# Kernel tuning notes

Measured on AMD Instinct MI355X. Metric: run time of the kernel, lower is better.

The kernel has to match this reference:

```python
import jax, jax.numpy as jnp
import numpy as np

D = 256
N_CELL = 100000
N_NET = 50000
E = 300000
EPS = 1e-5


def _agg_mean(src_feat, edge_index, num_dst):
    # edge_index[0]=src, edge_index[1]=dst; gather + segment-sum + degree-normalize
    src_idx, dst_idx = edge_index[0], edge_index[1]
    summed = jax.ops.segment_sum(src_feat[src_idx], dst_idx, num_segments=num_dst)
    deg = jax.ops.segment_sum(jnp.ones((src_idx.shape[0], 1), src_feat.dtype), dst_idx, num_segments=num_dst)
    return summed / jnp.maximum(deg, 1.0)


def _mlp(x, w1, b1, w2, b2):
    return jax.nn.relu(x @ w1 + b1) @ w2 + b2


def _layernorm(x, g, b):
    mu = jnp.mean(x, axis=-1, keepdims=True)
    var = jnp.var(x, axis=-1, keepdims=True)
    return (x - mu) * jax.lax.rsqrt(var + EPS) * g + b


def setup_inputs() -> dict:
    key = jax.random.key(0)
    ks = jax.random.split(key, 24)
    inp = {
        'cell_h': jax.random.normal(ks[0], (N_CELL, D), jnp.float32),
        'net_h': jax.random.normal(ks[1], (N_NET, D), jnp.float32),
        'cell_to_net_edge_index': jax.random.randint(ks[2], (2, E), 0, 50000),
        'net_to_cell_edge_index': jax.random.randint(ks[3], (2, E), 0, 50000),
        'cell_to_cell_edge_index': jax.random.randint(ks[4], (2, E), 0, 50000),
    }
    def lin(k, fin, fout):
        return jax.random.normal(k, (fin, fout), jnp.float32) * 0.02
    for i, name in enumerate(['c2n', 'n2c', 'c2c']):
        inp[name + '_w1'] = lin(ks[5 + 4 * i], 2 * D, D)
        inp[name + '_b1'] = jnp.zeros((D,), jnp.float32)
        inp[name + '_w2'] = lin(ks[6 + 4 * i], D, D)
        inp[name + '_b2'] = jnp.zeros((D,), jnp.float32)
    inp['net_ln_g'] = jnp.ones((D,), jnp.float32)
    inp['net_ln_b'] = jnp.zeros((D,), jnp.float32)
    inp['cell_ln_g'] = jnp.ones((D,), jnp.float32)
    inp['cell_ln_b'] = jnp.zeros((D,), jnp.float32)
    return inp


def reference(cell_h, net_h, cell_to_net_edge_index, net_to_cell_edge_index,
              cell_to_cell_edge_index,
              c2n_w1, c2n_b1, c2n_w2, c2n_b2,
              n2c_w1, n2c_b1, n2c_w2, n2c_b2,
              c2c_w1, c2c_b1, c2c_w2, c2c_b2,
              net_ln_g, net_ln_b, cell_ln_g, cell_ln_b):
    # cells -> nets
    msg_c2n = _agg_mean(cell_h, cell_to_net_edge_index, net_h.shape[0])
    net_h = _layernorm(net_h + _mlp(jnp.concatenate([net_h, msg_c2n], axis=-1),
                                    c2n_w1, c2n_b1, c2n_w2, c2n_b2),
                       net_ln_g, net_ln_b)
    # nets -> cells
    msg_n2c = _agg_mean(net_h, net_to_cell_edge_index, cell_h.shape[0])
    cell_h = cell_h + _mlp(jnp.concatenate([cell_h, msg_n2c], axis=-1),
                           n2c_w1, n2c_b1, n2c_w2, n2c_b2)
    # cells -> cells
    msg_c2c = _agg_mean(cell_h, cell_to_cell_edge_index, cell_h.shape[0])
    cell_h = cell_h + _mlp(jnp.concatenate([cell_h, msg_c2c], axis=-1),
                           c2c_w1, c2c_b1, c2c_w2, c2c_b2)
    cell_h = _layernorm(cell_h, cell_ln_g, cell_ln_b)
    return (cell_h, net_h)
```

## Files before the change

kernel.cpp:

```cpp
#include <hip/hip_runtime.h>
#include <stdint.h>

typedef unsigned short u16;
typedef short short8 __attribute__((ext_vector_type(8)));
typedef short short4v __attribute__((ext_vector_type(4)));
typedef float floatx4 __attribute__((ext_vector_type(4)));

#define D_FEAT 256

__device__ __forceinline__ u16 f2bf(float x){
  unsigned u = __float_as_uint(x);
  u += 0x7FFFu + ((u >> 16) & 1u);
  return (u16)(u >> 16);
}

__device__ __forceinline__ short8 pack8(float4 a, float4 b){
  short8 v;
  v[0]=(short)f2bf(a.x); v[1]=(short)f2bf(a.y); v[2]=(short)f2bf(a.z); v[3]=(short)f2bf(a.w);
  v[4]=(short)f2bf(b.x); v[5]=(short)f2bf(b.y); v[6]=(short)f2bf(b.z); v[7]=(short)f2bf(b.w);
  return v;
}

__global__ void conv_t_kernel(const float* __restrict__ w, u16* __restrict__ wt, int K, int N){
  int idx = blockIdx.x * 256 + threadIdx.x;
  if (idx >= K * N) return;
  int k = idx / N, n = idx - k * N;
  wt[(size_t)n * K + k] = f2bf(w[idx]);
}

__global__ void hist_kernel(const int* __restrict__ didx, int E, int* __restrict__ cnt){
  int e = blockIdx.x * 256 + threadIdx.x;
  if (e < E) atomicAdd(&cnt[didx[e]], 1);
}

__global__ void scan_block_kernel(const int* __restrict__ cnt, int* __restrict__ excl,
                                  int* __restrict__ bsums, int N){
  __shared__ int tmp[256];
  int t = threadIdx.x;
  int i = blockIdx.x * 256 + t;
  int v = (i < N) ? cnt[i] : 0;
  tmp[t] = v; __syncthreads();
#pragma unroll
  for (int o = 1; o < 256; o <<= 1){
    int x = (t >= o) ? tmp[t - o] : 0;
    __syncthreads();
    tmp[t] += x;
    __syncthreads();
  }
  if (i < N) excl[i] = tmp[t] - v;
  if (t == 255) bsums[blockIdx.x] = tmp[255];
}

__global__ void scan_bsums_kernel(int* __restrict__ bsums, int nb){
  __shared__ int tmp[512];
  int t = threadIdx.x;
  if (nb > 512){
    if (t == 0){
      int acc = 0;
      for (int i = 0; i < nb; i++){ int v = bsums[i]; bsums[i] = acc; acc += v; }
    }
    return;
  }
  int v = (t < nb) ? bsums[t] : 0;
  tmp[t] = v; __syncthreads();
#pragma unroll
  for (int o = 1; o < 512; o <<= 1){
    int x = (t >= o) ? tmp[t - o] : 0;
    __syncthreads();
    tmp[t] += x;
    __syncthreads();
  }
  if (t < nb) bsums[t] = tmp[t] - v;
}

__global__ void scan_add_kernel(int* __restrict__ excl, const int* __restrict__ bsums, int N){
  int i = blockIdx.x * 256 + threadIdx.x;
  if (i < N) excl[i] += bsums[blockIdx.x];
}

__global__ void fill_csr_kernel(const int* __restrict__ sidx, const int* __restrict__ didx, int E,
                                const int* __restrict__ row_start, int* __restrict__ fillc,
                                int* __restrict__ esrc){
  int e = blockIdx.x * 256 + threadIdx.x;
  if (e >= E) return;
  int d = didx[e];
  int pos = atomicAdd(&fillc[d], 1);
  esrc[row_start[d] + pos] = sidx[e];
}

__global__ void agg_mean_kernel(const float* __restrict__ feat, const int* __restrict__ row_start,
                                const int* __restrict__ cnt, const int* __restrict__ esrc,
                                u16* __restrict__ mean, int M){
  int row = blockIdx.x * 4 + (threadIdx.x >> 6);
  int lane = threadIdx.x & 63;
  if (row >= M) return;
  int beg = row_start[row], n = cnt[row];
  float4 a0 = {0.f,0.f,0.f,0.f}, a1 = {0.f,0.f,0.f,0.f};
  int j = 0;
  for (; j + 1 < n; j += 2){
    int s0 = esrc[beg + j], s1 = esrc[beg + j + 1];
    float4 v0 = ((const float4*)(feat + (size_t)s0 * D_FEAT))[lane];
    float4 v1 = ((const float4*)(feat + (size_t)s1 * D_FEAT))[lane];
    a0.x += v0.x; a0.y += v0.y; a0.z += v0.z; a0.w += v0.w;
    a1.x += v1.x; a1.y += v1.y; a1.z += v1.z; a1.w += v1.w;
  }
  if (j < n){
    int s0 = esrc[beg + j];
    float4 v0 = ((const float4*)(feat + (size_t)s0 * D_FEAT))[lane];
    a0.x += v0.x; a0.y += v0.y; a0.z += v0.z; a0.w += v0.w;
  }
  float inv = 1.0f / fmaxf((float)n, 1.0f);
  short4v o;
  o[0] = (short)f2bf((a0.x + a1.x) * inv);
  o[1] = (short)f2bf((a0.y + a1.y) * inv);
  o[2] = (short)f2bf((a0.z + a1.z) * inv);
  o[3] = (short)f2bf((a0.w + a1.w) * inv);
  ((short4v*)(mean + (size_t)row * D_FEAT))[lane] = o;
}

template<int HAS_LN>
__global__ __launch_bounds__(256, 3) void fused_mlp_kernel(
    const float* __restrict__ h, const u16* __restrict__ s,
    const u16* __restrict__ B1t, const float* __restrict__ b1,
    const u16* __restrict__ B2t, const float* __restrict__ b2,
    const float* __restrict__ resid,
    const float* __restrict__ lng, const float* __restrict__ lnb,
    float* __restrict__ out, int M)
{
  __shared__ __align__(16) char smem_raw[53248];
  short8* As8 = (short8*)smem_raw;
  short8* Bs8 = (short8*)(smem_raw + 4096);
  u16*    hid = (u16*)(smem_raw + 20480);
  float*  part = (float*)smem_raw;

  int tid = threadIdx.x;
  int wave = tid >> 6, lane = tid & 63;
  int half = lane >> 4, l16 = lane & 15;
  int wc = wave * 64;
  int row0 = blockIdx.x * 64;

  int rA = tid >> 2, uA = tid & 3;
  int rgA = row0 + rA;
  int aw_idx = (rA << 2) | (uA ^ (rA & 3));

  floatx4 acc[4][4];
  floatx4 zero4 = {0.f, 0.f, 0.f, 0.f};
#pragma unroll
  for (int i = 0; i < 4; i++)
#pragma unroll
    for (int j = 0; j < 4; j++) acc[i][j] = zero4;

  float4 pa0 = {0.f,0.f,0.f,0.f}, pa1 = {0.f,0.f,0.f,0.f};
  short8 ps = {0,0,0,0,0,0,0,0};
  short8 pbv[4];

  {
    int kk = uA * 8;
    if (rgA < M){
      const float* src = h + (size_t)rgA * 256 + kk;
      pa0 = ((const float4*)src)[0];
      pa1 = ((const float4*)src)[1];
    }
#pragma unroll
    for (int cc = 0; cc < 4; cc++){
      int c = tid + cc * 256;
      int r = c >> 2, u = c & 3;
      pbv[cc] = *(const short8*)(B1t + (size_t)r * 512 + u * 8);
    }
  }

  for (int k0 = 0; k0 < 512; k0 += 32){
    {
      short8 va = {0,0,0,0,0,0,0,0};
      if (k0 < 256){ if (rgA < M) va = pack8(pa0, pa1); }
      else         { va = ps; }
      As8[aw_idx] = va;
    }
#pragma unroll
    for (int cc = 0; cc < 4; cc++){
      int c = tid + cc * 256;
      int r = c >> 2, u = c & 3;
      Bs8[(r << 2) | (u ^ (r & 3))] = pbv[cc];
    }
    __syncthreads();

    if (k0 < 480){
      int k0n = k0 + 32;
      int kk = k0n + uA * 8;
      if (k0n < 256){
        if (rgA < M){
          const float* src = h + (size_t)rgA * 256 + kk;
          pa0 = ((const float4*)src)[0];
          pa1 = ((const float4*)src)[1];
        }
      } else {
        ps = (rgA < M) ? *(const short8*)(s + (size_t)rgA * 256 + (kk - 256))
                       : (short8){0,0,0,0,0,0,0,0};
      }
#pragma unroll
      for (int cc = 0; cc < 4; cc++){
        int c = tid + cc * 256;
        int r = c >> 2, u = c & 3;
        pbv[cc] = *(const short8*)(B1t + (size_t)r * 512 + k0n + u * 8);
      }
    }

    short8 af[4], bfr[4];
#pragma unroll
    for (int t = 0; t < 4; t++){
      int ra = t * 16 + l16;
      af[t] = As8[(ra << 2) | (half ^ (ra & 3))];
      int rb = wc + t * 16 + l16;
      bfr[t] = Bs8[(rb << 2) | (half ^ (rb & 3))];
    }
#pragma unroll
    for (int i = 0; i < 4; i++)
#pragma unroll
      for (int j = 0; j < 4; j++)
        acc[i][j] = __builtin_amdgcn_mfma_f32_16x16x32_bf16(af[i], bfr[j], acc[i][j], 0, 0, 0);
    __syncthreads();
  }

#pragma unroll
  for (int i = 0; i < 4; i++){
#pragma unroll
    for (int j = 0; j < 4; j++){
      int cg = wc + j * 16 + l16;
      float bv = b1[cg];
#pragma unroll
      for (int r = 0; r < 4; r++){
        int lr = i * 16 + half * 4 + r;
        int idx = lr * 256 + ((((cg >> 3) ^ (lr & 7)) << 3) | (cg & 7));
        hid[idx] = f2bf(fmaxf(acc[i][j][r] + bv, 0.0f));
      }
    }
  }

#pragma unroll
  for (int i = 0; i < 4; i++)
#pragma unroll
    for (int j = 0; j < 4; j++) acc[i][j] = zero4;

#pragma unroll
  for (int cc = 0; cc < 4; cc++){
    int c = tid + cc * 256;
    int r = c >> 2, u = c & 3;
    pbv[cc] = *(const short8*)(B2t + (size_t)r * 256 + u * 8);
  }

  for (int k0 = 0; k0 < 256; k0 += 32){
#pragma unroll
    for (int cc = 0; cc < 4; cc++){
      int c = tid + cc * 256;
      int r = c >> 2, u = c & 3;
      Bs8[(r << 2) | (u ^ (r & 3))] = pbv[cc];
    }
    __syncthreads();

    if (k0 < 224){
      int k0n = k0 + 32;
#pragma unroll
      for (int cc = 0; cc < 4; cc++){
        int c = tid + cc * 256;
        int r = c >> 2, u = c & 3;
        pbv[cc] = *(const short8*)(B2t + (size_t)r * 256 + k0n + u * 8);
      }
    }

    short8 af[4], bfr[4];
#pragma unroll
    for (int t = 0; t < 4; t++){
      int ra = t * 16 + l16;
      int chunkL = (k0 >> 3) + half;
      af[t] = *(const short8*)(hid + ra * 256 + ((chunkL ^ (ra & 7)) << 3));
      int rb = wc + t * 16 + l16;
      bfr[t] = Bs8[(rb << 2) | (half ^ (rb & 3))];
    }
#pragma unroll
    for (int i = 0; i < 4; i++)
#pragma unroll
      for (int j = 0; j < 4; j++)
        acc[i][j] = __builtin_amdgcn_mfma_f32_16x16x32_bf16(af[i], bfr[j], acc[i][j], 0, 0, 0);
    __syncthreads();
  }

#pragma unroll
  for (int i = 0; i < 4; i++){
#pragma unroll
    for (int j = 0; j < 4; j++){
      int cg = wc + j * 16 + l16;
      float bv = b2[cg];
#pragma unroll
      for (int r = 0; r < 4; r++){
        int lr = i * 16 + half * 4 + r;
        int rg = row0 + lr;
        float rv = (rg < M) ? resid[(size_t)rg * 256 + cg] : 0.0f;
        acc[i][j][r] = acc[i][j][r] + bv + rv;
      }
    }
  }

  if (HAS_LN){
#pragma unroll
    for (int i = 0; i < 4; i++){
#pragma unroll
      for (int r = 0; r < 4; r++){
        float s1 = 0.f, s2 = 0.f;
#pragma unroll
        for (int j = 0; j < 4; j++){
          float v = acc[i][j][r];
          s1 += v; s2 += v * v;
        }
#pragma unroll
        for (int m = 1; m < 16; m <<= 1){
          s1 += __shfl_xor(s1, m, 64);
          s2 += __shfl_xor(s2, m, 64);
        }
        if (l16 == 0){
          int lr = i * 16 + half * 4 + r;
          part[lr * 4 + wave]       = s1;
          part[256 + lr * 4 + wave] = s2;
        }
      }
    }
    __syncthreads();
#pragma unroll
    for (int i = 0; i < 4; i++){
#pragma unroll
      for (int r = 0; r < 4; r++){
        int lr = i * 16 + half * 4 + r;
        int rg = row0 + lr;
        float4 p1 = *(const float4*)(part + lr * 4);
        float4 p2 = *(const float4*)(part + 256 + lr * 4);
        float su = p1.x + p1.y + p1.z + p1.w;
        float sq = p2.x + p2.y + p2.z + p2.w;
        float mean = su * (1.0f / 256.0f);
        float var = sq * (1.0f / 256.0f) - mean * mean;
        float rs = rsqrtf(var + 1e-5f);
        if (rg < M){
#pragma unroll
          for (int j = 0; j < 4; j++){
            int cg = wc + j * 16 + l16;
            float vv = (acc[i][j][r] - mean) * rs * lng[cg] + lnb[cg];
            out[(size_t)rg * 256 + cg] = vv;
          }
        }
      }
    }
  } else {
#pragma unroll
    for (int i = 0; i < 4; i++){
#pragma unroll
      for (int r = 0; r < 4; r++){
        int lr = i * 16 + half * 4 + r;
        int rg = row0 + lr;
        if (rg < M){
#pragma unroll
          for (int j = 0; j < 4; j++){
            int cg = wc + j * 16 + l16;
            out[(size_t)rg * 256 + cg] = acc[i][j][r];
          }
        }
      }
    }
  }
}

static void run_agg(const float* feat, const int* edge, int E, int Ndst,
                    int* cnt, int* row_start, int* fillc, int* bsums, int* esrc,
                    u16* mean, hipStream_t stream){
  const int* sidx = edge;
  const int* didx = edge + E;
  hipMemsetAsync(cnt, 0, (size_t)Ndst * 4, stream);
  hipMemsetAsync(fillc, 0, (size_t)Ndst * 4, stream);
  int egrid = (E + 255) / 256;
  hist_kernel<<<egrid, 256, 0, stream>>>(didx, E, cnt);
  int nb = (Ndst + 255) / 256;
  scan_block_kernel<<<nb, 256, 0, stream>>>(cnt, row_start, bsums, Ndst);
  scan_bsums_kernel<<<1, 512, 0, stream>>>(bsums, nb);
  scan_add_kernel<<<nb, 256, 0, stream>>>(row_start, bsums, Ndst);
  fill_csr_kernel<<<egrid, 256, 0, stream>>>(sidx, didx, E, row_start, fillc, esrc);
  agg_mean_kernel<<<(Ndst + 3) / 4, 256, 0, stream>>>(feat, row_start, cnt, esrc, mean, Ndst);
}

extern "C" void kernel_launch(void* const* d_in, const int* in_sizes, int n_in,
                              void* d_out, int out_size, void* d_ws, size_t ws_size,
                              hipStream_t stream){
  const float* cell_h = (const float*)d_in[0];
  const float* net_h  = (const float*)d_in[1];
  const int* e_c2n = (const int*)d_in[2];
  const int* e_n2c = (const int*)d_in[3];
  const int* e_c2c = (const int*)d_in[4];
  const float* w1p[3] = {(const float*)d_in[5], (const float*)d_in[9],  (const float*)d_in[13]};
  const float* b1p[3] = {(const float*)d_in[6], (const float*)d_in[10], (const float*)d_in[14]};
  const float* w2p[3] = {(const float*)d_in[7], (const float*)d_in[11], (const float*)d_in[15]};
  const float* b2p[3] = {(const float*)d_in[8], (const float*)d_in[12], (const float*)d_in[16]};
  const float* net_g  = (const float*)d_in[17];
  const float* net_b  = (const float*)d_in[18];
  const float* cell_g = (const float*)d_in[19];
  const float* cell_b = (const float*)d_in[20];

  int n_cell = in_sizes[0] / 256;
  int n_net  = in_sizes[1] / 256;
  int E = in_sizes[2] / 2;

  float* cell_out = (float*)d_out;
  float* net_out  = (float*)d_out + (size_t)n_cell * 256;

  char* p = (char*)d_ws;
  u16* w1t[3]; u16* w2t[3];
  for (int i = 0; i < 3; i++){
    w1t[i] = (u16*)p; p += (size_t)512 * 256 * 2;
    w2t[i] = (u16*)p; p += (size_t)256 * 256 * 2;
  }
  u16* Mbuf = (u16*)p; p += (size_t)n_cell * 256 * 2;
  int n_pad = ((n_cell + 63) / 64) * 64;
  int* cnt       = (int*)p; p += (size_t)n_pad * 4;
  int* row_start = (int*)p; p += (size_t)n_pad * 4;
  int* fillc     = (int*)p; p += (size_t)n_pad * 4;
  int* bsums     = (int*)p; p += 1024 * 4;
  int* esrc      = (int*)p; p += (size_t)E * 4;

  for (int i = 0; i < 3; i++){
    conv_t_kernel<<<(512 * 256 + 255) / 256, 256, 0, stream>>>(w1p[i], w1t[i], 512, 256);
    conv_t_kernel<<<(256 * 256 + 255) / 256, 256, 0, stream>>>(w2p[i], w2t[i], 256, 256);
  }

  dim3 blk(256);

  run_agg(cell_h, e_c2n, E, n_net, cnt, row_start, fillc, bsums, esrc, Mbuf, stream);
  fused_mlp_kernel<1><<<dim3((n_net + 63) / 64), blk, 0, stream>>>(
      net_h, Mbuf, w1t[0], b1p[0], w2t[0], b2p[0], net_h, net_g, net_b, net_out, n_net);

  run_agg(net_out, e_n2c, E, n_cell, cnt, row_start, fillc, bsums, esrc, Mbuf, stream);
  fused_mlp_kernel<0><<<dim3((n_cell + 63) / 64), blk, 0, stream>>>(
      cell_h, Mbuf, w1t[1], b1p[1], w2t[1], b2p[1], cell_h, nullptr, nullptr, cell_out, n_cell);

  run_agg(cell_out, e_c2c, E, n_cell, cnt, row_start, fillc, bsums, esrc, Mbuf, stream);
  fused_mlp_kernel<1><<<dim3((n_cell + 63) / 64), blk, 0, stream>>>(
      cell_out, Mbuf, w1t[2], b1p[2], w2t[2], b2p[2], cell_out, cell_g, cell_b, cell_out, n_cell);
}
```

Before: 812.5 us.

## Double-buffer MLP weight tiles via direct global-to-LDS loads with pre-swizzled weights

Weights are now stored in a pre-swizzled per-K-step layout, so each 32-wide B tile can be copied straight into LDS with global_load_lds, skipping the register round trip. Both GEMM loops double-buffer the A and B tiles, dropping one barrier per step and overlapping the next tile's load with the current MFMAs. The LDS footprint grows to 64KB and launch bounds drop to 2 blocks per CU, so occupancy falls. The CSR fill also folds the fill counter initialisation into the scan-add kernel, which removes a memset and an indirect load.

```diff
diff --git a/kernel.cpp b/kernel.cpp
--- a/kernel.cpp
+++ b/kernel.cpp
@@ -21,11 +21,19 @@
   return v;
 }
 
-__global__ void conv_t_kernel(const float* __restrict__ w, u16* __restrict__ wt, int K, int N){
+__device__ __forceinline__ void gload16(const void* g, void* l){
+  __builtin_amdgcn_global_load_lds(
+      (const __attribute__((address_space(1))) unsigned int*)g,
+      (__attribute__((address_space(3))) unsigned int*)l, 16, 0, 0);
+}
+
+__global__ void conv_swz_kernel(const float* __restrict__ w, u16* __restrict__ wt, int K){
   int idx = blockIdx.x * 256 + threadIdx.x;
-  if (idx >= K * N) return;
-  int k = idx / N, n = idx - k * N;
-  wt[(size_t)n * K + k] = f2bf(w[idx]);
+  if (idx >= K * 256) return;
+  int k = idx >> 8, n = idx & 255;
+  int step = k >> 5, u = (k >> 3) & 3, e = k & 7;
+  int q = u ^ (n & 3);
+  wt[((size_t)step << 13) | (((n << 2) | q) << 3) | e] = f2bf(w[idx]);
 }
 
 __global__ void hist_kernel(const int* __restrict__ didx, int E, int* __restrict__ cnt){
@@ -73,19 +81,22 @@
   if (t < nb) bsums[t] = tmp[t] - v;
 }
 
-__global__ void scan_add_kernel(int* __restrict__ excl, const int* __restrict__ bsums, int N){
+__global__ void scan_add_kernel(int* __restrict__ excl, const int* __restrict__ bsums,
+                                int* __restrict__ fillc, int N){
   int i = blockIdx.x * 256 + threadIdx.x;
-  if (i < N) excl[i] += bsums[blockIdx.x];
+  if (i < N){
+    int v = excl[i] + bsums[blockIdx.x];
+    excl[i] = v;
+    fillc[i] = v;
+  }
 }
 
 __global__ void fill_csr_kernel(const int* __restrict__ sidx, const int* __restrict__ didx, int E,
-                                const int* __restrict__ row_start, int* __restrict__ fillc,
-                                int* __restrict__ esrc){
+                                int* __restrict__ fillc, int* __restrict__ esrc){
   int e = blockIdx.x * 256 + threadIdx.x;
   if (e >= E) return;
-  int d = didx[e];
-  int pos = atomicAdd(&fillc[d], 1);
-  esrc[row_start[d] + pos] = sidx[e];
+  int pos = atomicAdd(&fillc[didx[e]], 1);
+  esrc[pos] = sidx[e];
 }
 
 __global__ void agg_mean_kernel(const float* __restrict__ feat, const int* __restrict__ row_start,
@@ -119,19 +130,19 @@
 }
 
 template<int HAS_LN>
-__global__ __launch_bounds__(256, 3) void fused_mlp_kernel(
+__global__ __launch_bounds__(256, 2) void fused_mlp_kernel(
     const float* __restrict__ h, const u16* __restrict__ s,
-    const u16* __restrict__ B1t, const float* __restrict__ b1,
-    const u16* __restrict__ B2t, const float* __restrict__ b2,
+    const u16* __restrict__ B1g, const float* __restrict__ b1,
+    const u16* __restrict__ B2g, const float* __restrict__ b2,
     const float* __restrict__ resid,
     const float* __restrict__ lng, const float* __restrict__ lnb,
     float* __restrict__ out, int M)
 {
-  __shared__ __align__(16) char smem_raw[53248];
-  short8* As8 = (short8*)smem_raw;
-  short8* Bs8 = (short8*)(smem_raw + 4096);
-  u16*    hid = (u16*)(smem_raw + 20480);
-  float*  part = (float*)smem_raw;
+  __shared__ __align__(16) char smem[65536];
+  short8* Bs  = (short8*)smem;
+  u16*    hid = (u16*)(smem + 32768);
+  short8* As  = (short8*)(smem + 32768);
+  float*  part = (float*)smem;
 
   int tid = threadIdx.x;
   int wave = tid >> 6, lane = tid & 63;
@@ -141,7 +152,8 @@
 
   int rA = tid >> 2, uA = tid & 3;
   int rgA = row0 + rA;
-  int aw_idx = (rA << 2) | (uA ^ (rA & 3));
+  bool rAok = rgA < M;
+  int aw_slot = (rA << 2) | (uA ^ (rA & 3));
 
   floatx4 acc[4][4];
   floatx4 zero4 = {0.f, 0.f, 0.f, 0.f};
@@ -150,68 +162,65 @@
 #pragma unroll
     for (int j = 0; j < 4; j++) acc[i][j] = zero4;
 
+  short8 zero8 = {0,0,0,0,0,0,0,0};
   float4 pa0 = {0.f,0.f,0.f,0.f}, pa1 = {0.f,0.f,0.f,0.f};
-  short8 ps = {0,0,0,0,0,0,0,0};
-  short8 pbv[4];
-
-  {
-    int kk = uA * 8;
-    if (rgA < M){
-      const float* src = h + (size_t)rgA * 256 + kk;
-      pa0 = ((const float4*)src)[0];
-      pa1 = ((const float4*)src)[1];
-    }
-#pragma unroll
-    for (int cc = 0; cc < 4; cc++){
-      int c = tid + cc * 256;
-      int r = c >> 2, u = c & 3;
-      pbv[cc] = *(const short8*)(B1t + (size_t)r * 512 + u * 8);
-    }
-  }
-
+  short8 ps = zero8;
+
+#pragma unroll
+  for (int cc = 0; cc < 4; cc++){
+    int base = cc * 256 + wc;
+    gload16((const char*)B1g + ((size_t)(base + lane) << 4), Bs + base);
+  }
+  if (rAok){
+    const float* src = h + (size_t)rgA * 256 + uA * 8;
+    pa0 = ((const float4*)src)[0];
+    pa1 = ((const float4*)src)[1];
+  }
+  As[aw_slot] = rAok ? pack8(pa0, pa1) : zero8;
+  if (rAok){
+    const float* src = h + (size_t)rgA * 256 + 32 + uA * 8;
+    pa0 = ((const float4*)src)[0];
+    pa1 = ((const float4*)src)[1];
+  }
+  __syncthreads();
+
+  int cur = 0;
   for (int k0 = 0; k0 < 512; k0 += 32){
-    {
-      short8 va = {0,0,0,0,0,0,0,0};
-      if (k0 < 256){ if (rgA < M) va = pack8(pa0, pa1); }
-      else         { va = ps; }
-      As8[aw_idx] = va;
-    }
-#pragma unroll
-    for (int cc = 0; cc < 4; cc++){
-      int c = tid + cc * 256;
-      int r = c >> 2, u = c & 3;
-      Bs8[(r << 2) | (u ^ (r & 3))] = pbv[cc];
-    }
-    __syncthreads();
-
+    int nxt = cur ^ 1;
     if (k0 < 480){
-      int k0n = k0 + 32;
-      int kk = k0n + uA * 8;
-      if (k0n < 256){
-        if (rgA < M){
+      int k1 = k0 + 32;
+      int stepB = k1 >> 5;
+#pragma unroll
+      for (int cc = 0; cc < 4; cc++){
+        int base = cc * 256 + wc;
+        gload16((const char*)B1g + ((((size_t)stepB << 10) + base + lane) << 4),
+                Bs + (nxt << 10) + base);
+      }
+      {
+        short8 va = zero8;
+        if (k1 < 256){ if (rAok) va = pack8(pa0, pa1); }
+        else         { if (rAok) va = ps; }
+        As[(nxt << 8) + aw_slot] = va;
+      }
+      int k2 = k1 + 32;
+      if (k2 < 512 && rAok){
+        int kk = k2 + uA * 8;
+        if (k2 < 256){
           const float* src = h + (size_t)rgA * 256 + kk;
           pa0 = ((const float4*)src)[0];
           pa1 = ((const float4*)src)[1];
-        }
-      } else {
-        ps = (rgA < M) ? *(const short8*)(s + (size_t)rgA * 256 + (kk - 256))
-                       : (short8){0,0,0,0,0,0,0,0};
-      }
-#pragma unroll
-      for (int cc = 0; cc < 4; cc++){
-        int c = tid + cc * 256;
-        int r = c >> 2, u = c & 3;
-        pbv[cc] = *(const short8*)(B1t + (size_t)r * 512 + k0n + u * 8);
-      }
-    }
-
+        } else {
+          ps = *(const short8*)(s + (size_t)rgA * 256 + (kk - 256));
+        }
+      }
+    }
     short8 af[4], bfr[4];
 #pragma unroll
     for (int t = 0; t < 4; t++){
       int ra = t * 16 + l16;
-      af[t] = As8[(ra << 2) | (half ^ (ra & 3))];
+      af[t] = As[(cur << 8) + ((ra << 2) | (half ^ (ra & 3)))];
       int rb = wc + t * 16 + l16;
-      bfr[t] = Bs8[(rb << 2) | (half ^ (rb & 3))];
+      bfr[t] = Bs[(cur << 10) + ((rb << 2) | (half ^ (rb & 3)))];
     }
 #pragma unroll
     for (int i = 0; i < 4; i++)
@@ -219,8 +228,14 @@
       for (int j = 0; j < 4; j++)
         acc[i][j] = __builtin_amdgcn_mfma_f32_16x16x32_bf16(af[i], bfr[j], acc[i][j], 0, 0, 0);
     __syncthreads();
-  }
-
+    cur = nxt;
+  }
+
+#pragma unroll
+  for (int cc = 0; cc < 4; cc++){
+    int base = cc * 256 + wc;
+    gload16((const char*)B2g + ((size_t)(base + lane) << 4), Bs + base);
+  }
 #pragma unroll
   for (int i = 0; i < 4; i++){
 #pragma unroll
@@ -229,44 +244,30 @@
       float bv = b1[cg];
 #pragma unroll
       for (int r = 0; r < 4; r++){
-        int lr = i * 16 + half * 4 + r;
+        int lr = i * 16 + ((half & 1) ? 0 : 0) + half * 4 + r;
         int idx = lr * 256 + ((((cg >> 3) ^ (lr & 7)) << 3) | (cg & 7));
         hid[idx] = f2bf(fmaxf(acc[i][j][r] + bv, 0.0f));
       }
     }
   }
-
 #pragma unroll
   for (int i = 0; i < 4; i++)
 #pragma unroll
     for (int j = 0; j < 4; j++) acc[i][j] = zero4;
-
-#pragma unroll
-  for (int cc = 0; cc < 4; cc++){
-    int c = tid + cc * 256;
-    int r = c >> 2, u = c & 3;
-    pbv[cc] = *(const short8*)(B2t + (size_t)r * 256 + u * 8);
-  }
-
+  __syncthreads();
+
+  cur = 0;
   for (int k0 = 0; k0 < 256; k0 += 32){
-#pragma unroll
-    for (int cc = 0; cc < 4; cc++){
-      int c = tid + cc * 256;
-      int r = c >> 2, u = c & 3;
-      Bs8[(r << 2) | (u ^ (r & 3))] = pbv[cc];
-    }
-    __syncthreads();
-
+    int nxt = cur ^ 1;
     if (k0 < 224){
-      int k0n = k0 + 32;
+      int stepB = (k0 + 32) >> 5;
 #pragma unroll
       for (int cc = 0; cc < 4; cc++){
-        int c = tid + cc * 256;
-        int r = c >> 2, u = c & 3;
-        pbv[cc] = *(const short8*)(B2t + (size_t)r * 256 + k0n + u * 8);
-      }
-    }
-
+        int base = cc * 256 + wc;
+        gload16((const char*)B2g + ((((size_t)stepB << 10) + base + lane) << 4),
+                Bs + (nxt << 10) + base);
+      }
+    }
     short8 af[4], bfr[4];
 #pragma unroll
     for (int t = 0; t < 4; t++){
@@ -274,7 +275,7 @@
       int chunkL = (k0 >> 3) + half;
       af[t] = *(const short8*)(hid + ra * 256 + ((chunkL ^ (ra & 7)) << 3));
       int rb = wc + t * 16 + l16;
-      bfr[t] = Bs8[(rb << 2) | (half ^ (rb & 3))];
+      bfr[t] = Bs[(cur << 10) + ((rb << 2) | (half ^ (rb & 3)))];
     }
 #pragma unroll
     for (int i = 0; i < 4; i++)
@@ -282,6 +283,7 @@
       for (int j = 0; j < 4; j++)
         acc[i][j] = __builtin_amdgcn_mfma_f32_16x16x32_bf16(af[i], bfr[j], acc[i][j], 0, 0, 0);
     __syncthreads();
+    cur = nxt;
   }
 
 #pragma unroll
@@ -372,14 +374,13 @@
   const int* sidx = edge;
   const int* didx = edge + E;
   hipMemsetAsync(cnt, 0, (size_t)Ndst * 4, stream);
-  hipMemsetAsync(fillc, 0, (size_t)Ndst * 4, stream);
   int egrid = (E + 255) / 256;
   hist_kernel<<<egrid, 256, 0, stream>>>(didx, E, cnt);
   int nb = (Ndst + 255) / 256;
   scan_block_kernel<<<nb, 256, 0, stream>>>(cnt, row_start, bsums, Ndst);
   scan_bsums_kernel<<<1, 512, 0, stream>>>(bsums, nb);
-  scan_add_kernel<<<nb, 256, 0, stream>>>(row_start, bsums, Ndst);
-  fill_csr_kernel<<<egrid, 256, 0, stream>>>(sidx, didx, E, row_start, fillc, esrc);
+  scan_add_kernel<<<nb, 256, 0, stream>>>(row_start, bsums, fillc, Ndst);
+  fill_csr_kernel<<<egrid, 256, 0, stream>>>(sidx, didx, E, fillc, esrc);
   agg_mean_kernel<<<(Ndst + 3) / 4, 256, 0, stream>>>(feat, row_start, cnt, esrc, mean, Ndst);
 }
 
@@ -422,8 +423,8 @@
   int* esrc      = (int*)p; p += (size_t)E * 4;
 
   for (int i = 0; i < 3; i++){
-    conv_t_kernel<<<(512 * 256 + 255) / 256, 256, 0, stream>>>(w1p[i], w1t[i], 512, 256);
-    conv_t_kernel<<<(256 * 256 + 255) / 256, 256, 0, stream>>>(w2p[i], w2t[i], 256, 256);
+    conv_swz_kernel<<<(512 * 256 + 255) / 256, 256, 0, stream>>>(w1p[i], w1t[i], 512);
+    conv_swz_kernel<<<(256 * 256 + 255) / 256, 256, 0, stream>>>(w2p[i], w2t[i], 256);
   }
 
   dim3 blk(256);
```

Result: faster. 788.8 us (-2.9%).
